# Performance work log

Measured on AMD Instinct MI355X. Metric: run time of the kernel, lower is better.

The kernel has to match this reference:

```python
import jax, jax.numpy as jnp
import numpy as np

BS, SEQ, ML, DEPTH = 32, 50, 16, 4
NN = 2 ** DEPTH - 1          # 15 nodes per complete binary tree (heap layout)
VOCAB, EMB, ENC = 50000, 128, 128
GH = 32                      # bigru hidden per direction
NC = 100                     # num_concepts
LH = 128                     # LSTM hidden
LIN = 2 + 2 * GH + NC + 1    # 167 LSTM feature dim


def _gru_dir(x, Wx, Wh, bx, bh, reverse):
    # x: [B, T, I]; torch GRU gate order r,z,n
    B, H = x.shape[0], Wh.shape[1]
    xe = jnp.einsum('bti,gi->btg', x, Wx) + bx   # [B,T,3H]
    xs = jnp.swapaxes(xe, 0, 1)
    if reverse:
        xs = xs[::-1]
    def step(h, xt):
        gh = h @ Wh.T + bh
        r = jax.nn.sigmoid(xt[:, :H] + gh[:, :H])
        z = jax.nn.sigmoid(xt[:, H:2 * H] + gh[:, H:2 * H])
        n = jnp.tanh(xt[:, 2 * H:] + r * gh[:, 2 * H:])
        hn = (1.0 - z) * n + z * h
        return hn, hn
    _, hs = jax.lax.scan(step, jnp.zeros((B, H), x.dtype), xs)
    if reverse:
        hs = hs[::-1]
    return jnp.swapaxes(hs, 0, 1)


def _lstm(x, Wx, Wh, bx, bh):
    # x: [B, T, I]; torch LSTM gate order i,f,g,o
    B, H = x.shape[0], Wh.shape[1]
    xe = jnp.einsum('bti,gi->btg', x, Wx) + bx   # [B,T,4H]
    def step(carry, xt):
        h, c = carry
        g = xt + h @ Wh.T + bh
        i = jax.nn.sigmoid(g[:, :H])
        f = jax.nn.sigmoid(g[:, H:2 * H])
        gg = jnp.tanh(g[:, 2 * H:3 * H])
        o = jax.nn.sigmoid(g[:, 3 * H:])
        c = f * c + i * gg
        h = o * jnp.tanh(c)
        return (h, c), h
    h0 = (jnp.zeros((B, H), x.dtype), jnp.zeros((B, H), x.dtype))
    _, hs = jax.lax.scan(step, h0, jnp.swapaxes(xe, 0, 1))
    return jnp.swapaxes(hs, 0, 1)


def setup_inputs() -> dict:
    key = jax.random.key(0)
    ks = jax.random.split(key, 24)
    p = {}
    p['p_id'] = jax.random.randint(ks[0], (BS, SEQ), 0, 1000)
    p['c_id'] = jax.random.randint(ks[1], (BS, SEQ), 0, NC)
    p['ast_tokens'] = jax.random.randint(ks[2], (BS, SEQ, ML, NN), 0, VOCAB)
    p['target_c'] = jax.nn.one_hot(jax.random.randint(ks[3], (BS, SEQ), 0, NC + 1), NC + 1, dtype=jnp.float32)
    p['c_embed'] = jax.random.normal(ks[4], (BS, SEQ, NC + 1), jnp.float32)
    p['cur_result'] = jax.random.normal(ks[5], (BS, SEQ, 2), jnp.float32)
    p['result'] = (jax.random.uniform(ks[6], (BS * SEQ,)) < 0.5).astype(jnp.float32)
    p['emb'] = jax.random.normal(ks[7], (VOCAB, EMB), jnp.float32) * 0.02
    p['Wc_w'] = jax.random.normal(ks[8], (ENC, EMB), jnp.float32) / np.sqrt(EMB)
    p['Wc_b'] = jnp.zeros((ENC,), jnp.float32)
    p['gru_WxF'] = jax.random.normal(ks[9], (3 * GH, ENC), jnp.float32) / np.sqrt(ENC)
    p['gru_WhF'] = jax.random.normal(ks[10], (3 * GH, GH), jnp.float32) / np.sqrt(GH)
    p['gru_bxF'] = jnp.zeros((3 * GH,), jnp.float32)
    p['gru_bhF'] = jnp.zeros((3 * GH,), jnp.float32)
    p['gru_WxB'] = jax.random.normal(ks[11], (3 * GH, ENC), jnp.float32) / np.sqrt(ENC)
    p['gru_WhB'] = jax.random.normal(ks[12], (3 * GH, GH), jnp.float32) / np.sqrt(GH)
    p['gru_bxB'] = jnp.zeros((3 * GH,), jnp.float32)
    p['gru_bhB'] = jnp.zeros((3 * GH,), jnp.float32)
    p['lstm_Wx'] = jax.random.normal(ks[13], (4 * LH, LIN), jnp.float32) / np.sqrt(LIN)
    p['lstm_Wh'] = jax.random.normal(ks[14], (4 * LH, LH), jnp.float32) / np.sqrt(LH)
    p['lstm_bx'] = jnp.zeros((4 * LH,), jnp.float32)
    p['lstm_bh'] = jnp.zeros((4 * LH,), jnp.float32)
    p['pred_w'] = jax.random.normal(ks[15], (NC + 1, LH), jnp.float32) / np.sqrt(LH)
    p['pred_b'] = jnp.zeros((NC + 1,), jnp.float32)
    return p


def reference(p_id, c_id, ast_tokens, target_c, c_embed, cur_result, result,
              emb, Wc_w, Wc_b,
              gru_WxF, gru_WhF, gru_bxF, gru_bhF,
              gru_WxB, gru_WhB, gru_bxB, gru_bhB,
              lstm_Wx, lstm_Wh, lstm_bx, lstm_bh,
              pred_w, pred_b):
    # BatchTreeEncoder: per-node W_c(emb(tok)), subtree-sum via bottom-up heap, max over nodes
    e = emb[ast_tokens] @ Wc_w.T + Wc_b          # [BS,SEQ,ML,NN,ENC]
    s = e
    for lvl in range(DEPTH - 2, -1, -1):          # bottom-up over fixed tree levels
        par = np.arange(2 ** lvl - 1, 2 ** (lvl + 1) - 1)
        s = s.at[..., par, :].add(s[..., 2 * par + 1, :] + s[..., 2 * par + 2, :])
    tree_enc = jnp.max(s, axis=3)                 # [BS,SEQ,ML,ENC]
    x = tree_enc.reshape(BS * SEQ, ML, ENC)
    hf = _gru_dir(x, gru_WxF, gru_WhF, gru_bxF, gru_bhF, False)
    hb = _gru_dir(x, gru_WxB, gru_WhB, gru_bxB, gru_bhB, True)
    gout = jnp.concatenate([hf, hb], axis=-1)     # [BS*SEQ, ML, 64]
    code = jnp.max(gout, axis=1).reshape(BS, SEQ, 2 * GH)  # max_pool1d over time
    lin = jnp.concatenate([c_embed, code, cur_result], axis=-1)  # [BS,SEQ,LIN]
    lout = _lstm(lin, lstm_Wx, lstm_Wh, lstm_bx, lstm_bh)         # [BS,SEQ,LH]
    pred = lout.reshape(BS * SEQ, LH) @ pred_w.T + pred_b         # [BS*SEQ, NC+1]
    tc = target_c.reshape(BS * SEQ, NC + 1)
    p1 = jnp.sum(pred * tc, axis=-1)              # bmm(pred, target_c)
    ncon = jnp.sum(tc, axis=-1)
    m = (ncon > 0).astype(pred.dtype)
    fp = p1 / jnp.maximum(ncon, 1.0)
    bce = jnp.maximum(fp, 0.0) - fp * result + jnp.log1p(jnp.exp(-jnp.abs(fp)))
    loss = jnp.sum(bce * m) / jnp.maximum(jnp.sum(m), 1.0)
    return loss, jax.nn.sigmoid(fp) * m, result * m
```

## Files before the change

kernel.cpp:

```cpp
#include <hip/hip_runtime.h>
#include <hip/hip_bf16.h>
#include <math.h>

#define BS 32
#define SEQ 50
#define ML 16
#define NN 15
#define NTREE (BS*SEQ*ML)
#define NROW (BS*SEQ)
#define VOCAB 50000
#define EMB 128
#define ENC 128
#define GH 32
#define NC 100
#define LH 128
#define LIN_D 167

typedef float f32x4 __attribute__((ext_vector_type(4)));
typedef short s16x8 __attribute__((ext_vector_type(8)));
typedef unsigned int u32;
typedef u32 u32x4v __attribute__((ext_vector_type(4)));

#define LOG2E 1.4426950408889634f
__device__ __forceinline__ float fsig(float x) {
  return __builtin_amdgcn_rcpf(1.f + __builtin_amdgcn_exp2f(-LOG2E * x));
}
__device__ __forceinline__ float ftanh(float x) {
  return 2.f * __builtin_amdgcn_rcpf(
             1.f + __builtin_amdgcn_exp2f(-2.f * LOG2E * x)) - 1.f;
}
__device__ __forceinline__ u32 pkbf(float x, float y) {
  u32 a = __float_as_uint(x), b = __float_as_uint(y);
  a = (a + 0x7FFFu + ((a >> 16) & 1u)) >> 16;
  b = (b + 0x7FFFu + ((b >> 16) & 1u)) >> 16;
  return a | (b << 16);
}
__device__ __forceinline__ unsigned short f2bf(float x) {
  u32 a = __float_as_uint(x);
  return (unsigned short)((a + 0x7FFFu + ((a >> 16) & 1u)) >> 16);
}
#define MFMA __builtin_amdgcn_mfma_f32_16x16x32_bf16

__global__ __launch_bounds__(256) void gemm_mfma(
    const float* __restrict__ A, const u32* __restrict__ Bpk,
    const float* __restrict__ bias, void* __restrict__ Cout,
    int M, int N, int out_bf16) {
  int w = threadIdx.x >> 6, lane = threadIdx.x & 63;
  int R0 = blockIdx.x * 64 + w * 16;
  int r = R0 + (lane & 15);
  int rm = (r < M) ? r : (M - 1);
  const float* Ar = A + (size_t)rm * 128 + (lane >> 4) * 8;
  s16x8 a0, a1, a2, a3;
  {
#define LDA(AF, KT) { \
    float4 f0 = *(const float4*)(Ar + KT * 32); \
    float4 f1 = *(const float4*)(Ar + KT * 32 + 4); \
    u32x4v q = {pkbf(f0.x, f0.y), pkbf(f0.z, f0.w), \
                pkbf(f1.x, f1.y), pkbf(f1.z, f1.w)}; \
    AF = __builtin_bit_cast(s16x8, q); }
    LDA(a0, 0) LDA(a1, 1) LDA(a2, 2) LDA(a3, 3)
#undef LDA
  }
  const u32x4v* Bp = (const u32x4v*)Bpk;
  for (int c = 0; c < N; c += 64) {
    f32x4 acc0, acc1, acc2, acc3;
    {
      float b0 = bias ? bias[c + (lane & 15)]      : 0.f;
      float b1 = bias ? bias[c + 16 + (lane & 15)] : 0.f;
      float b2 = bias ? bias[c + 32 + (lane & 15)] : 0.f;
      float b3 = bias ? bias[c + 48 + (lane & 15)] : 0.f;
      acc0 = (f32x4){b0, b0, b0, b0}; acc1 = (f32x4){b1, b1, b1, b1};
      acc2 = (f32x4){b2, b2, b2, b2}; acc3 = (f32x4){b3, b3, b3, b3};
    }
    int fbase = (c >> 4) * 4;
#define DONT(ACC, NT) { \
    s16x8 bf0 = __builtin_bit_cast(s16x8, Bp[(size_t)(fbase + NT * 4 + 0) * 64 + lane]); \
    s16x8 bf1 = __builtin_bit_cast(s16x8, Bp[(size_t)(fbase + NT * 4 + 1) * 64 + lane]); \
    s16x8 bf2 = __builtin_bit_cast(s16x8, Bp[(size_t)(fbase + NT * 4 + 2) * 64 + lane]); \
    s16x8 bf3 = __builtin_bit_cast(s16x8, Bp[(size_t)(fbase + NT * 4 + 3) * 64 + lane]); \
    ACC = MFMA(a0, bf0, ACC, 0, 0, 0); ACC = MFMA(a1, bf1, ACC, 0, 0, 0); \
    ACC = MFMA(a2, bf2, ACC, 0, 0, 0); ACC = MFMA(a3, bf3, ACC, 0, 0, 0); }
    DONT(acc0, 0) DONT(acc1, 1) DONT(acc2, 2) DONT(acc3, 3)
#undef DONT
    int colb = c + (lane & 15);
    int rowb = R0 + (lane >> 4) * 4;
#define STNT(ACC, NT) \
    _Pragma("unroll") \
    for (int j = 0; j < 4; j++) { \
      int row = rowb + j; \
      if (row < M) { \
        if (out_bf16) ((unsigned short*)Cout)[(size_t)row * N + colb + NT * 16] = f2bf(ACC[j]); \
        else ((float*)Cout)[(size_t)row * N + colb + NT * 16] = ACC[j]; \
      } \
    }
    STNT(acc0, 0) STNT(acc1, 1) STNT(acc2, 2) STNT(acc3, 3)
#undef STNT
  }
}

__global__ __launch_bounds__(256) void gemm_mfma_bfA(
    const unsigned short* __restrict__ Ab, const u32* __restrict__ Bpk,
    const float* __restrict__ bias, float* __restrict__ Cout,
    int M, int N) {
  int w = threadIdx.x >> 6, lane = threadIdx.x & 63;
  int R0 = blockIdx.x * 64 + w * 16;
  int r = R0 + (lane & 15);
  int rm = (r < M) ? r : (M - 1);
  const unsigned short* Ar = Ab + (size_t)rm * 128 + (lane >> 4) * 8;
  s16x8 a0 = *(const s16x8*)(Ar + 0);
  s16x8 a1 = *(const s16x8*)(Ar + 32);
  s16x8 a2 = *(const s16x8*)(Ar + 64);
  s16x8 a3 = *(const s16x8*)(Ar + 96);
  const u32x4v* Bp = (const u32x4v*)Bpk;
  for (int c = 0; c < N; c += 64) {
    f32x4 acc0, acc1, acc2, acc3;
    {
      float b0 = bias[c + (lane & 15)];
      float b1 = bias[c + 16 + (lane & 15)];
      float b2 = bias[c + 32 + (lane & 15)];
      float b3 = bias[c + 48 + (lane & 15)];
      acc0 = (f32x4){b0, b0, b0, b0}; acc1 = (f32x4){b1, b1, b1, b1};
      acc2 = (f32x4){b2, b2, b2, b2}; acc3 = (f32x4){b3, b3, b3, b3};
    }
    int fbase = (c >> 4) * 4;
#define DONT(ACC, NT) { \
    s16x8 bf0 = __builtin_bit_cast(s16x8, Bp[(size_t)(fbase + NT * 4 + 0) * 64 + lane]); \
    s16x8 bf1 = __builtin_bit_cast(s16x8, Bp[(size_t)(fbase + NT * 4 + 1) * 64 + lane]); \
    s16x8 bf2 = __builtin_bit_cast(s16x8, Bp[(size_t)(fbase + NT * 4 + 2) * 64 + lane]); \
    s16x8 bf3 = __builtin_bit_cast(s16x8, Bp[(size_t)(fbase + NT * 4 + 3) * 64 + lane]); \
    ACC = MFMA(a0, bf0, ACC, 0, 0, 0); ACC = MFMA(a1, bf1, ACC, 0, 0, 0); \
    ACC = MFMA(a2, bf2, ACC, 0, 0, 0); ACC = MFMA(a3, bf3, ACC, 0, 0, 0); }
    DONT(acc0, 0) DONT(acc1, 1) DONT(acc2, 2) DONT(acc3, 3)
#undef DONT
    int colb = c + (lane & 15);
    int rowb = R0 + (lane >> 4) * 4;
#define STNT(ACC, NT) \
    _Pragma("unroll") \
    for (int j = 0; j < 4; j++) { \
      int row = rowb + j; \
      if (row < M) Cout[(size_t)row * N + colb + NT * 16] = ACC[j]; \
    }
    STNT(acc0, 0) STNT(acc1, 1) STNT(acc2, 2) STNT(acc3, 3)
#undef STNT
  }
}

__device__ __forceinline__ float lin_at(const float* __restrict__ ce,
    const float* __restrict__ co, const float* __restrict__ cu,
    int row, int k) {
  if (k < 101) return ce[row * 101 + k];
  if (k < 165) return co[row * 64 + (k - 101)];
  if (k < 167) return cu[row * 2 + (k - 165)];
  return 0.f;
}

__global__ __launch_bounds__(256) void gemm_lin(
    const float* __restrict__ c_embed, const float* __restrict__ code,
    const float* __restrict__ cur, const u32* __restrict__ Bpk,
    const float* __restrict__ bias, float* __restrict__ Cout) {
  int w = threadIdx.x >> 6, lane = threadIdx.x & 63;
  int R0 = blockIdx.x * 64 + w * 16;
  int r = R0 + (lane & 15);
  s16x8 a[6];
  #pragma unroll
  for (int kt = 0; kt < 6; kt++) {
    int k0 = kt * 32 + (lane >> 4) * 8;
    float f[8];
    #pragma unroll
    for (int j = 0; j < 8; j++) f[j] = lin_at(c_embed, code, cur, r, k0 + j);
    u32x4v q = {pkbf(f[0], f[1]), pkbf(f[2], f[3]),
                pkbf(f[4], f[5]), pkbf(f[6], f[7])};
    a[kt] = __builtin_bit_cast(s16x8, q);
  }
  const u32x4v* Bp = (const u32x4v*)Bpk;
  for (int c = 0; c < 512; c += 64) {
    f32x4 acc[4];
    #pragma unroll
    for (int nt = 0; nt < 4; nt++) {
      float bv = bias[c + nt * 16 + (lane & 15)];
      acc[nt] = (f32x4){bv, bv, bv, bv};
    }
    int fbase = (c >> 4) * 6;
    #pragma unroll
    for (int nt = 0; nt < 4; nt++) {
      #pragma unroll
      for (int kt = 0; kt < 6; kt++) {
        s16x8 bf = __builtin_bit_cast(s16x8,
            Bp[(size_t)(fbase + nt * 6 + kt) * 64 + lane]);
        acc[nt] = MFMA(a[kt], bf, acc[nt], 0, 0, 0);
      }
    }
    int colb = c + (lane & 15);
    int rowb = R0 + (lane >> 4) * 4;
    #pragma unroll
    for (int nt = 0; nt < 4; nt++)
      #pragma unroll
      for (int j = 0; j < 4; j++)
        Cout[(size_t)(rowb + j) * 512 + colb + nt * 16] = acc[nt][j];
  }
}

__global__ __launch_bounds__(256) void k_prep(const float* __restrict__ WxF,
    const float* __restrict__ WxB, const float* __restrict__ bxF,
    const float* __restrict__ bxB, const float* __restrict__ lstm_Wx,
    const float* __restrict__ lstm_Wh, const float* __restrict__ Wc_w,
    float* __restrict__ ball, u32* __restrict__ Wcpk,
    u32* __restrict__ Wallpk, u32* __restrict__ Wxpk, u32* __restrict__ Wpk) {
  int i = blockIdx.x * 256 + threadIdx.x;
  if (i < 96) ball[i] = bxF[i];
  else if (i < 192) ball[i] = bxB[i - 96];
  if (i < 8192) {
    int fg = i >> 8, l = (i >> 2) & 63, p = i & 3;
    int nt = fg >> 2, kt = fg & 3;
    int n = nt * 16 + (l & 15);
    int k = kt * 32 + (l >> 4) * 8 + 2 * p;
    Wcpk[i] = pkbf(Wc_w[n * 128 + k], Wc_w[n * 128 + k + 1]);
  }
  if (i < 12288) {
    int fg = i >> 8, l = (i >> 2) & 63, p = i & 3;
    int nt = fg >> 2, kt = fg & 3;
    int n = nt * 16 + (l & 15);
    int k = kt * 32 + (l >> 4) * 8 + 2 * p;
    float v0 = (n < 96) ? WxF[n * 128 + k]     : WxB[(n - 96) * 128 + k];
    float v1 = (n < 96) ? WxF[n * 128 + k + 1] : WxB[(n - 96) * 128 + k + 1];
    Wallpk[i] = pkbf(v0, v1);
  }
  if (i < 49152) {
    int fg = i >> 8, l = (i >> 2) & 63, p = i & 3;
    int nt = fg / 6, kt = fg % 6;
    int n = nt * 16 + (l & 15);
    int k = kt * 32 + (l >> 4) * 8 + 2 * p;
    float v0 = (k < LIN_D)     ? lstm_Wx[n * LIN_D + k]     : 0.f;
    float v1 = (k + 1 < LIN_D) ? lstm_Wx[n * LIN_D + k + 1] : 0.f;
    Wxpk[i] = pkbf(v0, v1);
  }
  if (i < 32768) {
    int fg = i >> 8, l = (i >> 2) & 63, p = i & 3;
    int w = fg >> 4, gt = (fg >> 2) & 3, kt = fg & 3;
    int n = 128 * gt + 16 * w + (l & 15);
    int k = 32 * kt + 8 * (l >> 4) + 2 * p;
    Wpk[i] = pkbf(lstm_Wh[n * 128 + k], lstm_Wh[n * 128 + k + 1]);
  }
}

__global__ __launch_bounds__(256) void k_tree(const int* __restrict__ ast,
    const u32* __restrict__ Epb, const float* __restrict__ Wc_b,
    unsigned short* __restrict__ x_bf) {
  int lt = threadIdx.x >> 7;
  int d  = threadIdx.x & 127;
  int tree = blockIdx.x * 2 + lt;
  __shared__ int toks[2][15];
  if (d < 15) toks[lt][d] = ast[(size_t)tree * 15 + d];
  __syncthreads();
  float e[15];
  int half = d >> 1;
  bool odd = (d & 1) != 0;
  #pragma unroll
  for (int n = 0; n < 15; n++) {
    u32 v = Epb[(size_t)toks[lt][n] * 64 + half];
    e[n] = __uint_as_float(odd ? (v & 0xFFFF0000u) : (v << 16));
  }
  float b = Wc_b[d];
  float s3 = e[3] + e[7] + e[8],  s4 = e[4] + e[9] + e[10];
  float s5 = e[5] + e[11] + e[12], s6 = e[6] + e[13] + e[14];
  float s1 = e[1] + s3 + s4, s2 = e[2] + s5 + s6;
  float s0 = e[0] + s1 + s2;
  float ml = fmaxf(fmaxf(fmaxf(e[7], e[8]), fmaxf(e[9], e[10])),
                   fmaxf(fmaxf(e[11], e[12]), fmaxf(e[13], e[14]))) + b;
  float mm = fmaxf(fmaxf(s3, s4), fmaxf(s5, s6)) + 3.f * b;
  float mt = fmaxf(s1, s2) + 7.f * b;
  float m = fmaxf(fmaxf(ml, mm), fmaxf(mt, s0 + 15.f * b));
  x_bf[(size_t)tree * 128 + d] = f2bf(m);
}

__global__ __launch_bounds__(128) void k_gru(const float* __restrict__ xe_all,
    const float* __restrict__ WhF, const float* __restrict__ WhB,
    const float* __restrict__ bhF, const float* __restrict__ bhB,
    float* __restrict__ code) {
  int bsq = blockIdx.x >> 1, dir = blockIdx.x & 1;
  int g = threadIdx.x;
  __shared__ float whs[96 * 32];
  __shared__ float h_lds[32];
  __shared__ float rz[64];
  __shared__ float nn[32];
  const float* Wh = dir ? WhB : WhF;
  const float* bh = dir ? bhB : bhF;
  for (int i = g; i < 96 * 32; i += 128) whs[i] = Wh[i];
  if (g < 32) h_lds[g] = 0.f;
  __syncthreads();
  float w[32]; float bhv = 0.f, mxv = -1e30f;
  if (g < 96) {
    #pragma unroll
    for (int j = 0; j < 32; j++) w[j] = whs[g * 32 + j];
    bhv = bh[g];
  }
  for (int s = 0; s < 16; s++) {
    int t = dir ? (15 - s) : s;
    const float* xe = xe_all + ((size_t)(bsq * 16 + t)) * 192 + dir * 96;
    float gh = bhv, xv = 0.f;
    if (g < 96) {
      xv = xe[g];
      #pragma unroll
      for (int j = 0; j < 32; j++) gh += w[j] * h_lds[j];
    }
    if (g < 64) rz[g] = fsig(xv + gh);
    __syncthreads();
    if (g >= 64 && g < 96) nn[g - 64] = ftanh(xv + rz[g - 64] * gh);
    __syncthreads();
    if (g < 32) {
      float z = rz[g + 32];
      float hn = (1.f - z) * nn[g] + z * h_lds[g];
      mxv = fmaxf(mxv, hn);
      h_lds[g] = hn;
    }
    __syncthreads();
  }
  if (g < 32) code[(size_t)bsq * 64 + dir * 32 + g] = mxv;
}

__global__ __launch_bounds__(512) void k_lstm(
    const float* __restrict__ xeL, const u32* __restrict__ Wpk,
    const float* __restrict__ bh, float* __restrict__ lout) {
  __shared__ float xl[SEQ * 512];
  __shared__ float hh[SEQ * 128];
  __shared__ s16x8 hl8[16];
  short* hls = (short*)hl8;
  int b = blockIdx.x, t = threadIdx.x;
  int w = t >> 6, lane = t & 63;
  const float* xrow = xeL + (size_t)b * SEQ * 512;
  #pragma unroll 5
  for (int i = t; i < SEQ * 512; i += 512) xl[i] = xrow[i];
  const s16x8* WB = (const s16x8*)Wpk + (size_t)w * 16 * 64 + lane;
  s16x8 B00 = WB[0*64],  B01 = WB[1*64],  B02 = WB[2*64],  B03 = WB[3*64];
  s16x8 B10 = WB[4*64],  B11 = WB[5*64],  B12 = WB[6*64],  B13 = WB[7*64];
  s16x8 B20 = WB[8*64],  B21 = WB[9*64],  B22 = WB[10*64], B23 = WB[11*64];
  s16x8 B30 = WB[12*64], B31 = WB[13*64], B32 = WB[14*64], B33 = WB[15*64];

  int u16 = 16 * w + lane;
  float bh0 = 0, bh1 = 0, bh2 = 0, bh3 = 0;
  if (lane < 16) {
    bh0 = bh[u16]; bh1 = bh[128 + u16]; bh2 = bh[256 + u16]; bh3 = bh[384 + u16];
  }
  float c = 0.f;
  if (t < 128) hls[t] = 0;
  __syncthreads();
  const s16x8 zz = {0, 0, 0, 0, 0, 0, 0, 0};
  const bool arow = (lane & 15) == 0;
  const int asel = lane >> 4;
  for (int step = 0; step < SEQ; step++) {
    s16x8 a0 = arow ? hl8[asel]      : zz;
    s16x8 a1 = arow ? hl8[4 + asel]  : zz;
    s16x8 a2 = arow ? hl8[8 + asel]  : zz;
    s16x8 a3 = arow ? hl8[12 + asel] : zz;
    f32x4 acc0 = {0, 0, 0, 0}, acc1 = {0, 0, 0, 0};
    f32x4 acc2 = {0, 0, 0, 0}, acc3 = {0, 0, 0, 0};
    if (lane < 16) {
      const float* xs = xl + step * 512;
      acc0[0] = xs[u16]       + bh0;
      acc1[0] = xs[128 + u16] + bh1;
      acc2[0] = xs[256 + u16] + bh2;
      acc3[0] = xs[384 + u16] + bh3;
    }
    acc0 = MFMA(a0, B00, acc0, 0, 0, 0); acc0 = MFMA(a1, B01, acc0, 0, 0, 0);
    acc0 = MFMA(a2, B02, acc0, 0, 0, 0); acc0 = MFMA(a3, B03, acc0, 0, 0, 0);
    acc1 = MFMA(a0, B10, acc1, 0, 0, 0); acc1 = MFMA(a1, B11, acc1, 0, 0, 0);
    acc1 = MFMA(a2, B12, acc1, 0, 0, 0); acc1 = MFMA(a3, B13, acc1, 0, 0, 0);
    acc2 = MFMA(a0, B20, acc2, 0, 0, 0); acc2 = MFMA(a1, B21, acc2, 0, 0, 0);
    acc2 = MFMA(a2, B22, acc2, 0, 0, 0); acc2 = MFMA(a3, B23, acc2, 0, 0, 0);
    acc3 = MFMA(a0, B30, acc3, 0, 0, 0); acc3 = MFMA(a1, B31, acc3, 0, 0, 0);
    acc3 = MFMA(a2, B32, acc3, 0, 0, 0); acc3 = MFMA(a3, B33, acc3, 0, 0, 0);
    if (lane < 16) {
      float iv = fsig(acc0[0]);
      float fv = fsig(acc1[0]);
      float gv = ftanh(acc2[0]);
      float ov = fsig(acc3[0]);
      c = fv * c + iv * gv;
      float h = ov * ftanh(c);
      hh[step * 128 + u16] = h;
      hls[u16] = (short)f2bf(h);
    }
    __syncthreads();
  }
  float* lo = lout + (size_t)b * SEQ * 128;
  #pragma unroll 4
  for (int i = t; i < SEQ * 128; i += 512) lo[i] = hh[i];
}

__global__ __launch_bounds__(128) void k_pred(const float* __restrict__ lout,
    const float* __restrict__ pred_w, const float* __restrict__ pred_b,
    const float* __restrict__ tc, const float* __restrict__ result,
    float* __restrict__ out, float* __restrict__ fpbuf, float* __restrict__ mbuf) {
  int row = blockIdx.x; int k = threadIdx.x;
  __shared__ float tcs[101];
  __shared__ float r1[128], r2[128], r3[128];
  if (k < 101) tcs[k] = tc[(size_t)row * 101 + k];
  __syncthreads();
  float lk = lout[(size_t)row * 128 + k];
  float acc = 0.f;
  for (int c = 0; c < 101; c++) acc += tcs[c] * pred_w[c * 128 + k];
  float v = acc * lk;
  float pb = (k < 101) ? tcs[k] * pred_b[k] : 0.f;
  float nc = (k < 101) ? tcs[k] : 0.f;
  r1[k] = v; r2[k] = pb; r3[k] = nc;
  __syncthreads();
  for (int st = 64; st > 0; st >>= 1) {
    if (k < st) { r1[k] += r1[k + st]; r2[k] += r2[k + st]; r3[k] += r3[k + st]; }
    __syncthreads();
  }
  if (k == 0) {
    float ncon = r3[0];
    float m = (ncon > 0.f) ? 1.f : 0.f;
    float fp = (r1[0] + r2[0]) / fmaxf(ncon, 1.f);
    fpbuf[row] = fp; mbuf[row] = m;
    out[1 + row] = m / (1.f + expf(-fp));
    out[1 + NROW + row] = result[row] * m;
  }
}

__global__ __launch_bounds__(256) void k_loss(const float* __restrict__ fpbuf,
    const float* __restrict__ mbuf, const float* __restrict__ result,
    float* __restrict__ out) {
  __shared__ float sb[256], sm[256];
  int k = threadIdx.x;
  float ab = 0.f, am = 0.f;
  for (int r = k; r < NROW; r += 256) {
    float fp = fpbuf[r], m = mbuf[r], res = result[r];
    float bce = fmaxf(fp, 0.f) - fp * res + log1pf(expf(-fabsf(fp)));
    ab += bce * m; am += m;
  }
  sb[k] = ab; sm[k] = am;
  __syncthreads();
  for (int st = 128; st > 0; st >>= 1) {
    if (k < st) { sb[k] += sb[k + st]; sm[k] += sm[k + st]; }
    __syncthreads();
  }
  if (k == 0) out[0] = sb[0] / fmaxf(sm[0], 1.f);
}

extern "C" void kernel_launch(void* const* d_in, const int* in_sizes, int n_in,
                              void* d_out, int out_size, void* d_ws, size_t ws_size,
                              hipStream_t stream) {
  (void)in_sizes; (void)n_in; (void)out_size; (void)ws_size;
  const int*   ast      = (const int*)  d_in[2];
  const float* target_c = (const float*)d_in[3];
  const float* c_embed  = (const float*)d_in[4];
  const float* cur_res  = (const float*)d_in[5];
  const float* result   = (const float*)d_in[6];
  const float* emb      = (const float*)d_in[7];
  const float* Wc_w     = (const float*)d_in[8];
  const float* Wc_b     = (const float*)d_in[9];
  const float* gru_WxF  = (const float*)d_in[10];
  const float* gru_WhF  = (const float*)d_in[11];
  const float* gru_bxF  = (const float*)d_in[12];
  const float* gru_bhF  = (const float*)d_in[13];
  const float* gru_WxB  = (const float*)d_in[14];
  const float* gru_WhB  = (const float*)d_in[15];
  const float* gru_bxB  = (const float*)d_in[16];
  const float* gru_bhB  = (const float*)d_in[17];
  const float* lstm_Wx  = (const float*)d_in[18];
  const float* lstm_Wh  = (const float*)d_in[19];
  const float* lstm_bx  = (const float*)d_in[20];
  const float* lstm_bh  = (const float*)d_in[21];
  const float* pred_w   = (const float*)d_in[22];
  const float* pred_b   = (const float*)d_in[23];
  float* out = (float*)d_out;

  float* W = (float*)d_ws;
  u32*   Epb    = (u32*)W;
  unsigned short* x_bf = (unsigned short*)(W + 3200000);
  float* xe_all = W + 4838400;
  float* code   = W + 9753600;
  float* xeL    = W + 9856000;
  float* lout   = W + 10675200;
  float* fpbuf  = W + 10880000;
  float* mbuf   = W + 10881600;
  u32*   Wcpk   = (u32*)(W + 10883200);
  u32*   Wallpk = (u32*)(W + 10891392);
  u32*   Wxpk   = (u32*)(W + 10903680);
  u32*   Wpk    = (u32*)(W + 10952832);
  float* ball   = W + 10985600;

  k_prep<<<192, 256, 0, stream>>>(gru_WxF, gru_WxB, gru_bxF, gru_bxB, lstm_Wx,
                                  lstm_Wh, Wc_w, ball, Wcpk, Wallpk, Wxpk, Wpk);
  gemm_mfma<<<782, 256, 0, stream>>>(emb, Wcpk, nullptr, Epb, VOCAB, 128, 1);
  k_tree<<<NTREE / 2, 256, 0, stream>>>(ast, Epb, Wc_b, x_bf);
  gemm_mfma_bfA<<<400, 256, 0, stream>>>(x_bf, Wallpk, ball, xe_all, NTREE, 192);
  k_gru<<<NROW * 2, 128, 0, stream>>>(xe_all, gru_WhF, gru_WhB, gru_bhF, gru_bhB, code);
  gemm_lin<<<25, 256, 0, stream>>>(c_embed, code, cur_res, Wxpk, lstm_bx, xeL);
  k_lstm<<<BS, 512, 0, stream>>>(xeL, Wpk, lstm_bh, lout);
  k_pred<<<NROW, 128, 0, stream>>>(lout, pred_w, pred_b, target_c, result,
                                   out, fpbuf, mbuf);
  k_loss<<<1, 256, 0, stream>>>(fpbuf, mbuf, result, out);
}
```

Measured before the change: 139.1 us.

## Move GRU recurrence onto MFMA per wave and add one-hot fast path in pred

```diff
diff --git a/kernel.cpp b/kernel.cpp
--- a/kernel.cpp
+++ b/kernel.cpp
@@ -204,8 +204,10 @@
     const float* __restrict__ WxB, const float* __restrict__ bxF,
     const float* __restrict__ bxB, const float* __restrict__ lstm_Wx,
     const float* __restrict__ lstm_Wh, const float* __restrict__ Wc_w,
+    const float* __restrict__ gru_WhF, const float* __restrict__ gru_WhB,
     float* __restrict__ ball, u32* __restrict__ Wcpk,
-    u32* __restrict__ Wallpk, u32* __restrict__ Wxpk, u32* __restrict__ Wpk) {
+    u32* __restrict__ Wallpk, u32* __restrict__ Wxpk, u32* __restrict__ Wpk,
+    u32* __restrict__ Wgpk) {
   int i = blockIdx.x * 256 + threadIdx.x;
   if (i < 96) ball[i] = bxF[i];
   else if (i < 192) ball[i] = bxB[i - 96];
@@ -240,6 +242,14 @@
     int n = 128 * gt + 16 * w + (l & 15);
     int k = 32 * kt + 8 * (l >> 4) + 2 * p;
     Wpk[i] = pkbf(lstm_Wh[n * 128 + k], lstm_Wh[n * 128 + k + 1]);
+  }
+  if (i < 3072) {
+    int fg = i >> 8, l = (i >> 2) & 63, p = i & 3;
+    int dir = fg / 6, nt = fg % 6;
+    int n = nt * 16 + (l & 15);
+    int k = (l >> 4) * 8 + 2 * p;
+    const float* Wh = dir ? gru_WhB : gru_WhF;
+    Wgpk[i] = pkbf(Wh[n * 32 + k], Wh[n * 32 + k + 1]);
   }
 }
 
@@ -273,49 +283,65 @@
   x_bf[(size_t)tree * 128 + d] = f2bf(m);
 }
 
-__global__ __launch_bounds__(128) void k_gru(const float* __restrict__ xe_all,
-    const float* __restrict__ WhF, const float* __restrict__ WhB,
-    const float* __restrict__ bhF, const float* __restrict__ bhB,
-    float* __restrict__ code) {
-  int bsq = blockIdx.x >> 1, dir = blockIdx.x & 1;
-  int g = threadIdx.x;
-  __shared__ float whs[96 * 32];
-  __shared__ float h_lds[32];
-  __shared__ float rz[64];
-  __shared__ float nn[32];
-  const float* Wh = dir ? WhB : WhF;
+__global__ __launch_bounds__(256) void k_gru(const float* __restrict__ xe_all,
+    const u32* __restrict__ Wgpk, const float* __restrict__ bhF,
+    const float* __restrict__ bhB, float* __restrict__ code) {
+  __shared__ float xls[32 * 192];
+  __shared__ short hls[4][32];
+  int t = threadIdx.x, w = t >> 6, lane = t & 63;
+  int sq0 = blockIdx.x * 2;
+  const float* xb = xe_all + (size_t)sq0 * 16 * 192;
+  #pragma unroll 4
+  for (int i = t; i < 32 * 192; i += 256) xls[i] = xb[i];
+  int sql = w >> 1, dir = w & 1;
+  int seq = sq0 + sql;
+  const s16x8* BG = (const s16x8*)Wgpk + (size_t)dir * 6 * 64 + lane;
+  s16x8 G0 = BG[0], G1 = BG[64], G2 = BG[128];
+  s16x8 G3 = BG[192], G4 = BG[256], G5 = BG[320];
   const float* bh = dir ? bhB : bhF;
-  for (int i = g; i < 96 * 32; i += 128) whs[i] = Wh[i];
-  if (g < 32) h_lds[g] = 0.f;
-  __syncthreads();
-  float w[32]; float bhv = 0.f, mxv = -1e30f;
-  if (g < 96) {
-    #pragma unroll
-    for (int j = 0; j < 32; j++) w[j] = whs[g * 32 + j];
-    bhv = bh[g];
-  }
+  float bh0 = 0, bh1 = 0, bh2 = 0, bh3 = 0, bh4 = 0, bh5 = 0;
+  if (lane < 16) {
+    bh0 = bh[lane];      bh1 = bh[16 + lane]; bh2 = bh[32 + lane];
+    bh3 = bh[48 + lane]; bh4 = bh[64 + lane]; bh5 = bh[80 + lane];
+  }
+  float h0 = 0.f, h1 = 0.f, mx0 = -1e30f, mx1 = -1e30f;
+  hls[w][lane & 31] = 0;
+  __syncthreads();
+  const s16x8 zz = {0, 0, 0, 0, 0, 0, 0, 0};
+  const bool arow = (lane & 15) == 0;
+  const int aoff = (lane >> 4) * 8;
   for (int s = 0; s < 16; s++) {
-    int t = dir ? (15 - s) : s;
-    const float* xe = xe_all + ((size_t)(bsq * 16 + t)) * 192 + dir * 96;
-    float gh = bhv, xv = 0.f;
-    if (g < 96) {
-      xv = xe[g];
-      #pragma unroll
-      for (int j = 0; j < 32; j++) gh += w[j] * h_lds[j];
-    }
-    if (g < 64) rz[g] = fsig(xv + gh);
-    __syncthreads();
-    if (g >= 64 && g < 96) nn[g - 64] = ftanh(xv + rz[g - 64] * gh);
-    __syncthreads();
-    if (g < 32) {
-      float z = rz[g + 32];
-      float hn = (1.f - z) * nn[g] + z * h_lds[g];
-      mxv = fmaxf(mxv, hn);
-      h_lds[g] = hn;
-    }
-    __syncthreads();
-  }
-  if (g < 32) code[(size_t)bsq * 64 + dir * 32 + g] = mxv;
+    int tt = dir ? (15 - s) : s;
+    const float* xr = xls + (sql * 16 + tt) * 192 + dir * 96;
+    s16x8 a = arow ? *(const s16x8*)&hls[w][aoff] : zz;
+    f32x4 ac0 = {0,0,0,0}, ac1 = {0,0,0,0}, ac2 = {0,0,0,0};
+    f32x4 ac3 = {0,0,0,0}, ac4 = {0,0,0,0}, ac5 = {0,0,0,0};
+    float xn0 = 0.f, xn1 = 0.f;
+    if (lane < 16) {
+      ac0[0] = xr[lane] + bh0;      ac1[0] = xr[16 + lane] + bh1;
+      ac2[0] = xr[32 + lane] + bh2; ac3[0] = xr[48 + lane] + bh3;
+      ac4[0] = bh4;                 ac5[0] = bh5;
+      xn0 = xr[64 + lane];          xn1 = xr[80 + lane];
+    }
+    ac0 = MFMA(a, G0, ac0, 0, 0, 0); ac1 = MFMA(a, G1, ac1, 0, 0, 0);
+    ac2 = MFMA(a, G2, ac2, 0, 0, 0); ac3 = MFMA(a, G3, ac3, 0, 0, 0);
+    ac4 = MFMA(a, G4, ac4, 0, 0, 0); ac5 = MFMA(a, G5, ac5, 0, 0, 0);
+    if (lane < 16) {
+      float r0 = fsig(ac0[0]), r1 = fsig(ac1[0]);
+      float z0 = fsig(ac2[0]), z1 = fsig(ac3[0]);
+      float n0 = ftanh(xn0 + r0 * ac4[0]);
+      float n1 = ftanh(xn1 + r1 * ac5[0]);
+      h0 = (1.f - z0) * n0 + z0 * h0;
+      h1 = (1.f - z1) * n1 + z1 * h1;
+      mx0 = fmaxf(mx0, h0); mx1 = fmaxf(mx1, h1);
+      hls[w][lane]      = (short)f2bf(h0);
+      hls[w][16 + lane] = (short)f2bf(h1);
+    }
+  }
+  if (lane < 16) {
+    code[(size_t)seq * 64 + dir * 32 + lane]      = mx0;
+    code[(size_t)seq * 64 + dir * 32 + 16 + lane] = mx1;
+  }
 }
 
 __global__ __launch_bounds__(512) void k_lstm(
@@ -395,22 +421,44 @@
   __shared__ float r1[128], r2[128], r3[128];
   if (k < 101) tcs[k] = tc[(size_t)row * 101 + k];
   __syncthreads();
-  float lk = lout[(size_t)row * 128 + k];
-  float acc = 0.f;
-  for (int c = 0; c < 101; c++) acc += tcs[c] * pred_w[c * 128 + k];
-  float v = acc * lk;
-  float pb = (k < 101) ? tcs[k] * pred_b[k] : 0.f;
-  float nc = (k < 101) ? tcs[k] : 0.f;
-  r1[k] = v; r2[k] = pb; r3[k] = nc;
+  float nz = 0.f, ixs = 0.f, vs = 0.f;
+  if (k < 101 && tcs[k] != 0.f) { nz = 1.f; ixs = (float)k; vs = tcs[k]; }
+  r1[k] = nz; r2[k] = ixs; r3[k] = vs;
   __syncthreads();
   for (int st = 64; st > 0; st >>= 1) {
     if (k < st) { r1[k] += r1[k + st]; r2[k] += r2[k + st]; r3[k] += r3[k + st]; }
     __syncthreads();
   }
+  float cnt = r1[0], idxf = r2[0], ncon = r3[0];
+  __syncthreads();
+  float fp, m;
+  if (cnt == 1.f && ncon == 1.f) {
+    int cls = (int)idxf;
+    float v = lout[(size_t)row * 128 + k] * pred_w[cls * 128 + k];
+    r1[k] = v;
+    __syncthreads();
+    for (int st = 64; st > 0; st >>= 1) {
+      if (k < st) r1[k] += r1[k + st];
+      __syncthreads();
+    }
+    fp = r1[0] + pred_b[cls];
+    m = 1.f;
+  } else {
+    float lk = lout[(size_t)row * 128 + k];
+    float acc = 0.f;
+    for (int c = 0; c < 101; c++) acc += tcs[c] * pred_w[c * 128 + k];
+    float v = acc * lk;
+    float pb = (k < 101) ? tcs[k] * pred_b[k] : 0.f;
+    r1[k] = v; r2[k] = pb;
+    __syncthreads();
+    for (int st = 64; st > 0; st >>= 1) {
+      if (k < st) { r1[k] += r1[k + st]; r2[k] += r2[k + st]; }
+      __syncthreads();
+    }
+    m = (ncon > 0.f) ? 1.f : 0.f;
+    fp = (r1[0] + r2[0]) / fmaxf(ncon, 1.f);
+  }
   if (k == 0) {
-    float ncon = r3[0];
-    float m = (ncon > 0.f) ? 1.f : 0.f;
-    float fp = (r1[0] + r2[0]) / fmaxf(ncon, 1.f);
     fpbuf[row] = fp; mbuf[row] = m;
     out[1 + row] = m / (1.f + expf(-fp));
     out[1 + NROW + row] = result[row] * m;
@@ -479,13 +527,15 @@
   u32*   Wxpk   = (u32*)(W + 10903680);
   u32*   Wpk    = (u32*)(W + 10952832);
   float* ball   = W + 10985600;
+  u32*   Wgpk   = (u32*)(W + 10985792);
 
   k_prep<<<192, 256, 0, stream>>>(gru_WxF, gru_WxB, gru_bxF, gru_bxB, lstm_Wx,
-                                  lstm_Wh, Wc_w, ball, Wcpk, Wallpk, Wxpk, Wpk);
+                                  lstm_Wh, Wc_w, gru_WhF, gru_WhB,
+                                  ball, Wcpk, Wallpk, Wxpk, Wpk, Wgpk);
   gemm_mfma<<<782, 256, 0, stream>>>(emb, Wcpk, nullptr, Epb, VOCAB, 128, 1);
   k_tree<<<NTREE / 2, 256, 0, stream>>>(ast, Epb, Wc_b, x_bf);
   gemm_mfma_bfA<<<400, 256, 0, stream>>>(x_bf, Wallpk, ball, xe_all, NTREE, 192);
-  k_gru<<<NROW * 2, 128, 0, stream>>>(xe_all, gru_WhF, gru_WhB, gru_bhF, gru_bhB, code);
+  k_gru<<<NROW / 2, 256, 0, stream>>>(xe_all, Wgpk, gru_bhF, gru_bhB, code);
   gemm_lin<<<25, 256, 0, stream>>>(c_embed, code, cur_res, Wxpk, lstm_bx, xeL);
   k_lstm<<<BS, 512, 0, stream>>>(xeL, Wpk, lstm_bh, lout);
   k_pred<<<NROW, 128, 0, stream>>>(lout, pred_w, pred_b, target_c, result,
```

Measured after the change: 133.2 us, median of 2. -4.3%, faster.
